# Kernel tuning notes

Hardware: AMD Instinct MI355X
Metric: run time of the kernel (lower is better)

The kernel has to match this reference:

```python
import jax, jax.numpy as jnp
import numpy as np

EPS = 1e-5
NEG_SLOPE = 0.2  # PyG GATConv default leaky_relu slope


def group_norm(x, w, b, groups):
    # x: [N, C] treated as batch of N samples, GroupNorm over channel groups
    N, C = x.shape
    xg = x.reshape(N, groups, C // groups)
    mu = xg.mean(-1, keepdims=True)
    var = ((xg - mu) ** 2).mean(-1, keepdims=True)
    xn = ((xg - mu) / jnp.sqrt(var + EPS)).reshape(N, C)
    return xn * w + b


def gat_conv(x, src, dst, W, a_src, a_dst, bias, n_nodes):
    # PyG GATConv, heads=1, concat=False, self-loops already appended to src/dst
    h = x @ W.T                                    # [N, C]
    alpha_src = h @ a_src                          # [N]
    alpha_dst = h @ a_dst                          # [N]
    e = jax.nn.leaky_relu(alpha_src[src] + alpha_dst[dst], NEG_SLOPE)  # [E]
    # segment softmax over edges grouped by destination node
    m = jax.ops.segment_max(e, dst, num_segments=n_nodes)
    ex = jnp.exp(e - m[dst])
    s = jax.ops.segment_sum(ex, dst, num_segments=n_nodes)
    alpha = ex / (s[dst] + 1e-16)                  # [E]
    out = jax.ops.segment_sum(h[src] * alpha[:, None], dst, num_segments=n_nodes)
    return out + bias


def setup_inputs() -> dict:
    key = jax.random.key(0)
    ks = jax.random.split(key, 32)
    N, E = 40000, 640000
    C_IN, C_OUT = 256, 512
    H = C_OUT // 2  # 256

    def xavier(k, shape):
        fan_in, fan_out = shape[1], shape[0]
        lim = np.sqrt(6.0 / (fan_in + fan_out))
        return jax.random.uniform(k, shape, jnp.float32, -lim, lim)

    inp = {
        "x": jax.random.normal(ks[0], (N, C_IN), jnp.float32),
        "edge_index": jax.random.randint(ks[1], (2, E), 0, N, jnp.int64),
        # pre_norm (GroupNorm(C_IN//8, C_IN))
        "pre_w": jnp.ones((C_IN,), jnp.float32),
        "pre_b": jnp.zeros((C_IN,), jnp.float32),
        # lin1: C_IN -> H
        "lin1_w": xavier(ks[2], (H, C_IN)),
        "lin1_b": jnp.zeros((H,), jnp.float32),
        "n1_w": jnp.ones((H,), jnp.float32),
        "n1_b": jnp.zeros((H,), jnp.float32),
        # GATConv 1 (H -> H, heads=1)
        "g1_w": xavier(ks[3], (H, H)),
        "g1_asrc": jax.random.normal(ks[4], (H,), jnp.float32) * 0.1,
        "g1_adst": jax.random.normal(ks[5], (H,), jnp.float32) * 0.1,
        "g1_b": jnp.zeros((H,), jnp.float32),
        "n2_w": jnp.ones((H,), jnp.float32),
        "n2_b": jnp.zeros((H,), jnp.float32),
        # GATConv 2
        "g2_w": xavier(ks[6], (H, H)),
        "g2_asrc": jax.random.normal(ks[7], (H,), jnp.float32) * 0.1,
        "g2_adst": jax.random.normal(ks[8], (H,), jnp.float32) * 0.1,
        "g2_b": jnp.zeros((H,), jnp.float32),
        "n3_w": jnp.ones((H,), jnp.float32),
        "n3_b": jnp.zeros((H,), jnp.float32),
        # lin2: H -> C_OUT
        "lin2_w": xavier(ks[9], (C_OUT, H)),
        "lin2_b": jnp.zeros((C_OUT,), jnp.float32),
        # skip_conv: C_IN -> C_OUT (in != out, so skip is applied)
        "skip_w": xavier(ks[10], (C_OUT, C_IN)),
        "skip_b": jnp.zeros((C_OUT,), jnp.float32),
    }
    return inp


def reference(x, edge_index, pre_w, pre_b, lin1_w, lin1_b, n1_w, n1_b,
              g1_w, g1_asrc, g1_adst, g1_b, n2_w, n2_b,
              g2_w, g2_asrc, g2_adst, g2_b, n3_w, n3_b,
              lin2_w, lin2_b, skip_w, skip_b):
    N, C_IN = x.shape
    H = lin1_w.shape[0]
    # add self loops (PyG GATConv default add_self_loops=True)
    loops = jnp.arange(N, dtype=edge_index.dtype)
    src = jnp.concatenate([edge_index[0], loops])
    dst = jnp.concatenate([edge_index[1], loops])

    y = jax.nn.elu(group_norm(x, pre_w, pre_b, C_IN // 8))
    y = y @ lin1_w.T + lin1_b
    y = jax.nn.elu(group_norm(y, n1_w, n1_b, H // 8))
    y = gat_conv(y, src, dst, g1_w, g1_asrc, g1_adst, g1_b, N)
    y = jax.nn.elu(group_norm(y, n2_w, n2_b, H // 8))
    y = gat_conv(y, src, dst, g2_w, g2_asrc, g2_adst, g2_b, N)
    y = jax.nn.elu(group_norm(y, n3_w, n3_b, H // 8))
    y = y @ lin2_w.T + lin2_b
    x_skip = x @ skip_w.T + skip_b  # in_channels != out_channels
    return x_skip + y
```

## Files before the change

### kernel.cpp

```cpp
#include <hip/hip_runtime.h>
#include <hip/hip_bf16.h>


typedef __bf16 bf16x8 __attribute__((ext_vector_type(8)));
typedef float floatx4 __attribute__((ext_vector_type(4)));

__device__ __forceinline__ __hip_bfloat16 f2b(float f) { return __float2bfloat16(f); }
__device__ __forceinline__ float bits2f(unsigned u) { return __uint_as_float(u << 16); }

__device__ __forceinline__ bf16x8 cvt8(const float* p) {
  float4 a = *(const float4*)p, b = *(const float4*)(p + 4);
  bf16x8 r;
  r[0] = (__bf16)a.x; r[1] = (__bf16)a.y; r[2] = (__bf16)a.z; r[3] = (__bf16)a.w;
  r[4] = (__bf16)b.x; r[5] = (__bf16)b.y; r[6] = (__bf16)b.z; r[7] = (__bf16)b.w;
  return r;
}

__global__ __launch_bounds__(256) void conv_w_k(
    const float* __restrict__ s0, const float* __restrict__ s1,
    const float* __restrict__ s2, const float* __restrict__ s3,
    const float* __restrict__ s4, __hip_bfloat16* __restrict__ d) {
  int i = (blockIdx.x * 256 + threadIdx.x) * 4;
  if (i >= 458752) return;
  const float* s; int off;
  if      (i < 65536)  { s = s0; off = 0; }
  else if (i < 131072) { s = s1; off = 65536; }
  else if (i < 196608) { s = s2; off = 131072; }
  else if (i < 327680) { s = s3; off = 196608; }
  else                 { s = s4; off = 327680; }
  float4 v = *(const float4*)(s + (i - off));
  union { ushort4 u; __hip_bfloat16 h[4]; } st;
  st.h[0] = f2b(v.x); st.h[1] = f2b(v.y); st.h[2] = f2b(v.z); st.h[3] = f2b(v.w);
  *(ushort4*)(d + i) = st.u;
}

__global__ __launch_bounds__(256) void gn_elu_k(
    const float* __restrict__ x, const float* __restrict__ w, const float* __restrict__ b,
    __hip_bfloat16* __restrict__ o, __hip_bfloat16* __restrict__ xb, int ng) {
  int g = blockIdx.x * 256 + threadIdx.x;
  if (g >= ng) return;
  int gi = g & 31;
  size_t basei = (size_t)g * 8;
  float4 u0 = *(const float4*)(x + basei), u1 = *(const float4*)(x + basei + 4);
  float f[8] = {u0.x, u0.y, u0.z, u0.w, u1.x, u1.y, u1.z, u1.w};
  if (xb) {
    union { uint4 u; __hip_bfloat16 h[8]; } xs;
#pragma unroll
    for (int i = 0; i < 8; i++) xs.h[i] = f2b(f[i]);
    *(uint4*)(xb + basei) = xs.u;
  }
  float mu = 0.f;
#pragma unroll
  for (int i = 0; i < 8; i++) mu += f[i];
  mu *= 0.125f;
  float var = 0.f;
#pragma unroll
  for (int i = 0; i < 8; i++) { float d = f[i] - mu; var += d * d; }
  float inv = rsqrtf(var * 0.125f + 1e-5f);
  union { uint4 u; __hip_bfloat16 h[8]; } st;
#pragma unroll
  for (int i = 0; i < 8; i++) {
    float vv = (f[i] - mu) * inv * w[gi * 8 + i] + b[gi * 8 + i];
    vv = (vv > 0.f) ? vv : (__expf(vv) - 1.f);
    st.h[i] = f2b(vv);
  }
  *(uint4*)(o + basei) = st.u;
}

template <int MODE>
__global__ __launch_bounds__(256, 3) void gemm_t(
    const __hip_bfloat16* __restrict__ A, const __hip_bfloat16* __restrict__ A2,
    const float* __restrict__ Af32,
    const __hip_bfloat16* __restrict__ W, const __hip_bfloat16* __restrict__ W2,
    const float* __restrict__ bias, const float* __restrict__ bias2,
    const float* __restrict__ gnw, const float* __restrict__ gnb,
    const float* __restrict__ avs, const float* __restrict__ avd,
    __hip_bfloat16* __restrict__ outB, float* __restrict__ outF,
    float* __restrict__ asrc, float* __restrict__ adst, int Nc, int Mreal) {
  const int tid = threadIdx.x;
  const int wn = tid >> 6, lane = tid & 63;
  const int l16 = lane & 15, quad = lane >> 4;
  const int rows0 = blockIdx.y * 64;
  const int col0 = blockIdx.x * 256;
  const int srow = tid >> 2, skc = (tid & 3) * 8;
  __shared__ __align__(16) __hip_bfloat16 sA[2][64 * 32];
  __shared__ __align__(16) __hip_bfloat16 sB[2][256 * 32];
  __shared__ float sRed[2][64][4];
  const int loA = tid * 8;

  floatx4 acc[4][4];
#pragma unroll
  for (int a = 0; a < 4; ++a)
#pragma unroll
    for (int b = 0; b < 4; ++b) acc[a][b] = (floatx4){0.f, 0.f, 0.f, 0.f};

  const int NK = (MODE >= 2) ? 16 : 8;
  uint4 pa, pb[4];
  pa = *(const uint4*)(A + (size_t)(rows0 + srow) * 256 + skc);
#pragma unroll
  for (int h = 0; h < 4; ++h)
    pb[h] = *(const uint4*)(W + (size_t)(col0 + srow + h * 64) * 256 + skc);
  *(uint4*)(&sA[0][loA]) = pa;
#pragma unroll
  for (int h = 0; h < 4; ++h) *(uint4*)(&sB[0][loA + h * 2048]) = pb[h];
  __syncthreads();

#pragma unroll
  for (int kt = 0; kt < NK; ++kt) {
    const int cur = kt & 1, nxt = cur ^ 1;
    const int ktn = kt + 1;
    const bool nsec = (MODE >= 2) && (ktn >= 8);
    const bool nstageA = (ktn < NK) && !(MODE == 3 && nsec);
    if (ktn < NK) {
      const int kkn = (ktn & 7) * 32;
      const __hip_bfloat16* Wb = nsec ? W2 : W;
      if (nstageA) {
        const __hip_bfloat16* Ab = (MODE == 2 && nsec) ? A2 : A;
        pa = *(const uint4*)(Ab + (size_t)(rows0 + srow) * 256 + kkn + skc);
      }
#pragma unroll
      for (int h = 0; h < 4; ++h)
        pb[h] = *(const uint4*)(Wb + (size_t)(col0 + srow + h * 64) * 256 + kkn + skc);
    }
    bf16x8 af[4], bfr[4];
    if (MODE == 3 && kt >= 8) {
      const int kk = (kt & 7) * 32;
#pragma unroll
      for (int ri = 0; ri < 4; ++ri) {
        int row = min(rows0 + ri * 16 + l16, Mreal - 1);
        af[ri] = cvt8(Af32 + (size_t)row * 256 + kk + quad * 8);
      }
    } else {
#pragma unroll
      for (int ri = 0; ri < 4; ++ri)
        af[ri] = *(const bf16x8*)(&sA[cur][(ri * 16 + l16) * 32 + quad * 8]);
    }
#pragma unroll
    for (int ci = 0; ci < 4; ++ci)
      bfr[ci] = *(const bf16x8*)(&sB[cur][(wn * 64 + ci * 16 + l16) * 32 + quad * 8]);
#pragma unroll
    for (int ri = 0; ri < 4; ++ri)
#pragma unroll
      for (int ci = 0; ci < 4; ++ci)
        acc[ri][ci] = __builtin_amdgcn_mfma_f32_16x16x32_bf16(af[ri], bfr[ci], acc[ri][ci], 0, 0, 0);
    if (ktn < NK) {
      if (nstageA) *(uint4*)(&sA[nxt][loA]) = pa;
#pragma unroll
      for (int h = 0; h < 4; ++h) *(uint4*)(&sB[nxt][loA + h * 2048]) = pb[h];
    }
    __syncthreads();
  }

  if (MODE == 0) {
#pragma unroll
    for (int ri = 0; ri < 4; ++ri)
#pragma unroll
      for (int ci = 0; ci < 4; ++ci) {
        int col = col0 + wn * 64 + ci * 16 + l16;
        float bs = bias[col], gw = gnw[col], gb = gnb[col];
#pragma unroll
        for (int i = 0; i < 4; ++i) {
          float v = acc[ri][ci][i] + bs;
          float s = v;
          s += __shfl_xor(s, 1, 64); s += __shfl_xor(s, 2, 64); s += __shfl_xor(s, 4, 64);
          float mu = s * 0.125f, d = v - mu;
          float q = d * d;
          q += __shfl_xor(q, 1, 64); q += __shfl_xor(q, 2, 64); q += __shfl_xor(q, 4, 64);
          float r = d * rsqrtf(q * 0.125f + 1e-5f) * gw + gb;
          r = (r > 0.f) ? r : (__expf(r) - 1.f);
          outB[(size_t)(rows0 + ri * 16 + quad * 4 + i) * 256 + col] = f2b(r);
        }
      }
  } else if (MODE == 1) {
#pragma unroll
    for (int ri = 0; ri < 4; ++ri) {
      float ps[4] = {0.f, 0.f, 0.f, 0.f}, pd[4] = {0.f, 0.f, 0.f, 0.f};
#pragma unroll
      for (int ci = 0; ci < 4; ++ci) {
        int col = col0 + wn * 64 + ci * 16 + l16;
        float wsv = avs[col], wdv = avd[col];
#pragma unroll
        for (int i = 0; i < 4; ++i) {
          float v = acc[ri][ci][i];
          outB[(size_t)(rows0 + ri * 16 + quad * 4 + i) * 256 + col] = f2b(v);
          ps[i] += v * wsv; pd[i] += v * wdv;
        }
      }
#pragma unroll
      for (int i = 0; i < 4; ++i) {
        ps[i] += __shfl_xor(ps[i], 1, 64); ps[i] += __shfl_xor(ps[i], 2, 64);
        ps[i] += __shfl_xor(ps[i], 4, 64); ps[i] += __shfl_xor(ps[i], 8, 64);
        pd[i] += __shfl_xor(pd[i], 1, 64); pd[i] += __shfl_xor(pd[i], 2, 64);
        pd[i] += __shfl_xor(pd[i], 4, 64); pd[i] += __shfl_xor(pd[i], 8, 64);
        if (l16 == 0) {
          int r = ri * 16 + quad * 4 + i;
          sRed[0][r][wn] = ps[i];
          sRed[1][r][wn] = pd[i];
        }
      }
    }
    __syncthreads();
    if (tid < 128) {
      int arr = tid >> 6, r = tid & 63;
      float v = sRed[arr][r][0] + sRed[arr][r][1] + sRed[arr][r][2] + sRed[arr][r][3];
      (arr ? adst : asrc)[rows0 + r] = v;
    }
  } else {
#pragma unroll
    for (int ri = 0; ri < 4; ++ri)
#pragma unroll
      for (int ci = 0; ci < 4; ++ci) {
        int col = col0 + wn * 64 + ci * 16 + l16;
        float bs = bias[col] + bias2[col];
#pragma unroll
        for (int i = 0; i < 4; ++i) {
          int row = rows0 + ri * 16 + quad * 4 + i;
          if (row < Mreal) outF[(size_t)row * Nc + col] = acc[ri][ci][i] + bs;
        }
      }
  }
}

__global__ void zero_k(int* p, int n) {
  int i = blockIdx.x * blockDim.x + threadIdx.x;
  if (i < n) p[i] = 0;
}

__global__ void count_deg_k(const int* __restrict__ ei, int E, int NN, int* __restrict__ counts) {
  int e = blockIdx.x * blockDim.x + threadIdx.x;
  if (e >= E + NN) return;
  int d = (e < E) ? ei[E + e] : (e - E);
  if ((unsigned)d >= (unsigned)NN) d = 0;
  atomicAdd(&counts[d], 1);
}

__global__ __launch_bounds__(1024) void scan_blk_k(const int* __restrict__ counts,
                                                   int* __restrict__ indptr,
                                                   int* __restrict__ bsums, int NN) {
  __shared__ int wsum[16];
  int t = threadIdx.x, idx = blockIdx.x * 1024 + t;
  int lane = t & 63, wid = t >> 6;
  int v = (idx < NN) ? counts[idx] : 0;
  int s = v;
#pragma unroll
  for (int off = 1; off < 64; off <<= 1) {
    int u = __shfl_up(s, off, 64);
    if (lane >= off) s += u;
  }
  if (lane == 63) wsum[wid] = s;
  __syncthreads();
  if (t == 0) {
    int run = 0;
#pragma unroll
    for (int i = 0; i < 16; i++) { int u = wsum[i]; wsum[i] = run; run += u; }
    bsums[blockIdx.x] = run;
  }
  __syncthreads();
  if (idx < NN) indptr[idx] = s - v + wsum[wid];
}

__global__ void scan_top_k(int* bsums, int nb) {
  if (threadIdx.x == 0) {
    int run = 0;
    for (int i = 0; i < nb; i++) { int t = bsums[i]; bsums[i] = run; run += t; }
  }
}

__global__ __launch_bounds__(1024) void scan_add_k(int* __restrict__ indptr, int* __restrict__ fill,
                                                   const int* __restrict__ bsums, int NN, int ET) {
  int idx = blockIdx.x * 1024 + threadIdx.x;
  if (idx < NN) {
    int v = indptr[idx] + bsums[blockIdx.x];
    indptr[idx] = v; fill[idx] = v;
  }
  if (idx == 0) indptr[NN] = ET;
}

__global__ void fill_csr_k(const int* __restrict__ ei, int E, int NN,
                           int* __restrict__ fill, int* __restrict__ csr, int ET) {
  int e = blockIdx.x * blockDim.x + threadIdx.x;
  if (e >= E + NN) return;
  int s, d;
  if (e < E) { s = ei[e]; d = ei[E + e]; } else { s = e - E; d = e - E; }
  if ((unsigned)d >= (unsigned)NN) d = 0;
  if ((unsigned)s >= (unsigned)NN) s = 0;
  int slot = atomicAdd(&fill[d], 1);
  if ((unsigned)slot < (unsigned)ET) csr[slot] = s;
}

__global__ __launch_bounds__(256) void gat_agg_gn_k(
    const __hip_bfloat16* __restrict__ h, const float* __restrict__ asrc,
    const float* __restrict__ adst, const int* __restrict__ indptr,
    const int* __restrict__ csr, const float* __restrict__ gbias,
    const float* __restrict__ gnw, const float* __restrict__ gnb,
    __hip_bfloat16* __restrict__ outp, int NN, int ET) {
  int n = blockIdx.x * 4 + (threadIdx.x >> 6);
  if (n >= NN) return;
  int lane = threadIdx.x & 63;
  int half = lane >> 5, l32 = lane & 31;
  int beg = indptr[n], end = indptr[n + 1];
  beg = max(0, min(beg, ET));
  end = max(beg, min(end, ET));
  int deg = end - beg;
  float adn = adst[n];
  float a[8] = {0.f, 0.f, 0.f, 0.f, 0.f, 0.f, 0.f, 0.f};
  float lw = 0.f;

  for (int cb = 0; cb < deg; cb += 64) {
    int j = cb + lane;
    int sid = 0; float w = 0.f;
    if (j < deg) {
      sid = csr[beg + j];
      if ((unsigned)sid >= (unsigned)NN) sid = 0;
      float e = asrc[sid] + adn;
      e = (e > 0.f) ? e : 0.2f * e;
      e = fminf(fmaxf(e, -60.f), 60.f);
      w = __expf(e);
    }
    lw += w;
    int cnt = min(64, deg - cb);
    for (int t = 0; t < cnt; t += 2) {
      int idx = t + half;
      int s = __shfl(sid, idx, 64);
      float wt = __shfl(w, idx, 64);
      uint4 u = *(const uint4*)(h + (size_t)s * 256 + l32 * 8);
      a[0] += wt * bits2f(u.x & 0xffffu); a[1] += wt * bits2f(u.x >> 16);
      a[2] += wt * bits2f(u.y & 0xffffu); a[3] += wt * bits2f(u.y >> 16);
      a[4] += wt * bits2f(u.z & 0xffffu); a[5] += wt * bits2f(u.z >> 16);
      a[6] += wt * bits2f(u.w & 0xffffu); a[7] += wt * bits2f(u.w >> 16);
    }
  }
#pragma unroll
  for (int i = 0; i < 8; ++i) a[i] += __shfl_xor(a[i], 32, 64);
#pragma unroll
  for (int m = 32; m >= 1; m >>= 1) lw += __shfl_xor(lw, m, 64);
  if (half == 0) {
    float inv = 1.f / (lw + 1e-16f);
    int c0 = l32 * 8;
    float v[8], mu = 0.f;
#pragma unroll
    for (int i = 0; i < 8; ++i) { v[i] = a[i] * inv + gbias[c0 + i]; mu += v[i]; }
    mu *= 0.125f;
    float q = 0.f;
#pragma unroll
    for (int i = 0; i < 8; ++i) { float d = v[i] - mu; q += d * d; }
    float rs = rsqrtf(q * 0.125f + 1e-5f);
    union { uint4 u; __hip_bfloat16 b[8]; } st;
#pragma unroll
    for (int i = 0; i < 8; ++i) {
      float r = (v[i] - mu) * rs * gnw[c0 + i] + gnb[c0 + i];
      r = (r > 0.f) ? r : (__expf(r) - 1.f);
      st.b[i] = f2b(r);
    }
    *(uint4*)(outp + (size_t)n * 256 + c0) = st.u;
  }
}

extern "C" void kernel_launch(void* const* d_in, const int* in_sizes, int n_in,
                              void* d_out, int out_size, void* d_ws, size_t ws_size,
                              hipStream_t stream) {
  const float* x      = (const float*)d_in[0];
  const int*   ei     = (const int*)d_in[1];
  const float* pre_w  = (const float*)d_in[2];
  const float* pre_b  = (const float*)d_in[3];
  const float* lin1_b = (const float*)d_in[5];
  const float* n1_w   = (const float*)d_in[6];
  const float* n1_b   = (const float*)d_in[7];
  const float* g1_as  = (const float*)d_in[9];
  const float* g1_ad  = (const float*)d_in[10];
  const float* g1_b   = (const float*)d_in[11];
  const float* n2_w   = (const float*)d_in[12];
  const float* n2_b   = (const float*)d_in[13];
  const float* g2_as  = (const float*)d_in[15];
  const float* g2_ad  = (const float*)d_in[16];
  const float* g2_b   = (const float*)d_in[17];
  const float* n3_w   = (const float*)d_in[18];
  const float* n3_b   = (const float*)d_in[19];
  const float* lin2_b = (const float*)d_in[21];
  const float* skip_b = (const float*)d_in[23];
  float* out = (float*)d_out;

  const int C_IN  = in_sizes[2];
  const int NN    = in_sizes[0] / C_IN;
  const int E     = in_sizes[1] / 2;
  const int ET    = E + NN;
  const int C_OUT = in_sizes[21];
  const int NP    = (NN + 127) & ~127;

  __hip_bfloat16* D0 = (__hip_bfloat16*)d_out;
  __hip_bfloat16* D1 = D0 + (size_t)NP * 256;

  char* basep = (char*)d_ws;
  size_t o = 0;
  auto alloc = [&](size_t bytes) { size_t r = o; o += (bytes + 255) & ~(size_t)255; return r; };
  __hip_bfloat16* Y      = (__hip_bfloat16*)(basep + alloc((size_t)NP * 256 * 2));
  __hip_bfloat16* Wcat   = (__hip_bfloat16*)(basep + alloc((size_t)458752 * 2));
  float*          asrc   = (float*)(basep + alloc((size_t)NP * 4));
  float*          adst   = (float*)(basep + alloc((size_t)NP * 4));
  int*            indptr = (int*)(basep + alloc((size_t)(NN + 1) * 4));
  int*            counts = (int*)(basep + alloc((size_t)NN * 4));
  int*            fill   = (int*)(basep + alloc((size_t)NN * 4));
  int*            bsums  = (int*)(basep + alloc(256));
  int*            csr    = (int*)(basep + alloc((size_t)ET * 4));
  size_t base_need = o;
  size_t xb_need = ((size_t)NP * 256 * 2 + 255) & ~(size_t)255;
  const bool use_xb = (ws_size >= base_need + xb_need);
  __hip_bfloat16* xb = use_xb ? (__hip_bfloat16*)(basep + alloc(xb_need)) : nullptr;

  __hip_bfloat16* Wlin1 = Wcat;
  __hip_bfloat16* Wg1   = Wcat + 65536;
  __hip_bfloat16* Wg2   = Wcat + 131072;
  __hip_bfloat16* Wlin2 = Wcat + 196608;
  __hip_bfloat16* Wskip = Wcat + 327680;

  dim3 blk(256);
  const int nb = (NN + 1023) / 1024;

  conv_w_k<<<(458752 / 4 + 255) / 256, blk, 0, stream>>>(
      (const float*)d_in[4], (const float*)d_in[8], (const float*)d_in[14],
      (const float*)d_in[20], (const float*)d_in[22], Wcat);
  zero_k<<<(NN + 255) / 256, blk, 0, stream>>>(counts, NN);
  count_deg_k<<<(ET + 255) / 256, blk, 0, stream>>>(ei, E, NN, counts);
  scan_blk_k<<<nb, 1024, 0, stream>>>(counts, indptr, bsums, NN);
  scan_top_k<<<1, 64, 0, stream>>>(bsums, nb);
  scan_add_k<<<nb, 1024, 0, stream>>>(indptr, fill, bsums, NN, ET);
  fill_csr_k<<<(ET + 255) / 256, blk, 0, stream>>>(ei, E, NN, fill, csr, ET);

  gn_elu_k<<<(NN * 32 + 255) / 256, blk, 0, stream>>>(x, pre_w, pre_b, D0, xb, NN * 32);
  gemm_t<0><<<dim3(1, NP / 64), blk, 0, stream>>>(D0, nullptr, nullptr, Wlin1, nullptr,
      lin1_b, nullptr, n1_w, n1_b, nullptr, nullptr, Y, nullptr, nullptr, nullptr, 256, NN);
  gemm_t<1><<<dim3(1, NP / 64), blk, 0, stream>>>(Y, nullptr, nullptr, Wg1, nullptr,
      nullptr, nullptr, nullptr, nullptr, g1_as, g1_ad, D0, nullptr, asrc, adst, 256, NN);
  gat_agg_gn_k<<<NN / 4, blk, 0, stream>>>(D0, asrc, adst, indptr, csr, g1_b, n2_w, n2_b, D1, NN, ET);
  gemm_t<1><<<dim3(1, NP / 64), blk, 0, stream>>>(D1, nullptr, nullptr, Wg2, nullptr,
      nullptr, nullptr, nullptr, nullptr, g2_as, g2_ad, D0, nullptr, asrc, adst, 256, NN);
  gat_agg_gn_k<<<NN / 4, blk, 0, stream>>>(D0, asrc, adst, indptr, csr, g2_b, n3_w, n3_b, Y, NN, ET);
  if (use_xb) {
    gemm_t<2><<<dim3(C_OUT / 256, NP / 64), blk, 0, stream>>>(Y, xb, nullptr, Wlin2, Wskip,
        lin2_b, skip_b, nullptr, nullptr, nullptr, nullptr, nullptr, out, nullptr, nullptr, C_OUT, NN);
  } else {
    gemm_t<3><<<dim3(C_OUT / 256, NP / 64), blk, 0, stream>>>(Y, nullptr, x, Wlin2, Wskip,
        lin2_b, skip_b, nullptr, nullptr, nullptr, nullptr, nullptr, out, nullptr, nullptr, C_OUT, NN);
  }
}
```

Baseline: 440.7 us.

## Split GAT aggregation into alpha pass and channel-blocked gather over blocked h layout

The GAT projection GEMM now writes h in a channel-blocked layout (8 blocks of 32 channels, each contiguous over rows). A new alpha kernel precomputes per-edge exp weights packed with source ids, plus the inverse softmax denominator per node. The aggregation kernel then runs one block per node group and channel block, gathering 64-byte rows so each channel slice stays small enough to stay cache-resident. This trades an extra kernel launch and an 8-byte-per-edge write and read for better gather locality, with GroupNorm reduced over 4-lane groups.

```diff
diff --git a/kernel.cpp b/kernel.cpp
--- a/kernel.cpp
+++ b/kernel.cpp
@@ -172,17 +172,20 @@
         }
       }
   } else if (MODE == 1) {
+    const int NPl = (Mreal + 127) & ~127;
 #pragma unroll
     for (int ri = 0; ri < 4; ++ri) {
       float ps[4] = {0.f, 0.f, 0.f, 0.f}, pd[4] = {0.f, 0.f, 0.f, 0.f};
 #pragma unroll
       for (int ci = 0; ci < 4; ++ci) {
         int col = col0 + wn * 64 + ci * 16 + l16;
+        int cbk = col >> 5, chin = col & 31;
         float wsv = avs[col], wdv = avd[col];
 #pragma unroll
         for (int i = 0; i < 4; ++i) {
           float v = acc[ri][ci][i];
-          outB[(size_t)(rows0 + ri * 16 + quad * 4 + i) * 256 + col] = f2b(v);
+          int row = rows0 + ri * 16 + quad * 4 + i;
+          outB[(size_t)cbk * NPl * 32 + (size_t)row * 32 + chin] = f2b(v);
           ps[i] += v * wsv; pd[i] += v * wdv;
         }
       }
@@ -288,71 +291,101 @@
   if ((unsigned)slot < (unsigned)ET) csr[slot] = s;
 }
 
-__global__ __launch_bounds__(256) void gat_agg_gn_k(
-    const __hip_bfloat16* __restrict__ h, const float* __restrict__ asrc,
-    const float* __restrict__ adst, const int* __restrict__ indptr,
-    const int* __restrict__ csr, const float* __restrict__ gbias,
-    const float* __restrict__ gnw, const float* __restrict__ gnb,
-    __hip_bfloat16* __restrict__ outp, int NN, int ET) {
+__global__ __launch_bounds__(256) void alpha_k(
+    const float* __restrict__ asrc, const float* __restrict__ adst,
+    const int* __restrict__ indptr, const int* __restrict__ csr,
+    unsigned long long* __restrict__ ew, float* __restrict__ lwinv, int NN, int ET) {
   int n = blockIdx.x * 4 + (threadIdx.x >> 6);
   if (n >= NN) return;
   int lane = threadIdx.x & 63;
-  int half = lane >> 5, l32 = lane & 31;
   int beg = indptr[n], end = indptr[n + 1];
   beg = max(0, min(beg, ET));
   end = max(beg, min(end, ET));
   int deg = end - beg;
   float adn = adst[n];
-  float a[8] = {0.f, 0.f, 0.f, 0.f, 0.f, 0.f, 0.f, 0.f};
   float lw = 0.f;
-
-  for (int cb = 0; cb < deg; cb += 64) {
-    int j = cb + lane;
-    int sid = 0; float w = 0.f;
+  for (int c0 = 0; c0 < deg; c0 += 64) {
+    int j = c0 + lane;
     if (j < deg) {
-      sid = csr[beg + j];
+      int sid = csr[beg + j];
       if ((unsigned)sid >= (unsigned)NN) sid = 0;
       float e = asrc[sid] + adn;
       e = (e > 0.f) ? e : 0.2f * e;
       e = fminf(fmaxf(e, -60.f), 60.f);
-      w = __expf(e);
-    }
-    lw += w;
-    int cnt = min(64, deg - cb);
-    for (int t = 0; t < cnt; t += 2) {
-      int idx = t + half;
-      int s = __shfl(sid, idx, 64);
-      float wt = __shfl(w, idx, 64);
-      uint4 u = *(const uint4*)(h + (size_t)s * 256 + l32 * 8);
-      a[0] += wt * bits2f(u.x & 0xffffu); a[1] += wt * bits2f(u.x >> 16);
-      a[2] += wt * bits2f(u.y & 0xffffu); a[3] += wt * bits2f(u.y >> 16);
-      a[4] += wt * bits2f(u.z & 0xffffu); a[5] += wt * bits2f(u.z >> 16);
-      a[6] += wt * bits2f(u.w & 0xffffu); a[7] += wt * bits2f(u.w >> 16);
-    }
-  }
-#pragma unroll
-  for (int i = 0; i < 8; ++i) a[i] += __shfl_xor(a[i], 32, 64);
+      float w = __expf(e);
+      ew[beg + j] = (unsigned)sid | ((unsigned long long)__float_as_uint(w) << 32);
+      lw += w;
+    }
+  }
 #pragma unroll
   for (int m = 32; m >= 1; m >>= 1) lw += __shfl_xor(lw, m, 64);
-  if (half == 0) {
-    float inv = 1.f / (lw + 1e-16f);
-    int c0 = l32 * 8;
-    float v[8], mu = 0.f;
-#pragma unroll
-    for (int i = 0; i < 8; ++i) { v[i] = a[i] * inv + gbias[c0 + i]; mu += v[i]; }
-    mu *= 0.125f;
-    float q = 0.f;
-#pragma unroll
-    for (int i = 0; i < 8; ++i) { float d = v[i] - mu; q += d * d; }
+  if (lane == 0) lwinv[n] = 1.f / (lw + 1e-16f);
+}
+
+__global__ __launch_bounds__(256) void gat_pass_k(
+    const __hip_bfloat16* __restrict__ hb, const unsigned long long* __restrict__ ew,
+    const float* __restrict__ lwinv, const int* __restrict__ indptr,
+    const float* __restrict__ gbias, const float* __restrict__ gnw,
+    const float* __restrict__ gnb, __hip_bfloat16* __restrict__ outp,
+    int NN, int NP, int ET) {
+  int bid = blockIdx.x;
+  int cbk = bid & 7;
+  int n = (bid >> 3) * 4 + (threadIdx.x >> 6);
+  if (n >= NN) return;
+  int lane = threadIdx.x & 63;
+  int qw = lane >> 4, l16 = lane & 15;
+  const __hip_bfloat16* hc = hb + (size_t)cbk * NP * 32;
+  int beg = indptr[n], end = indptr[n + 1];
+  beg = max(0, min(beg, ET));
+  end = max(beg, min(end, ET));
+  int deg = end - beg;
+  float a0 = 0.f, a1 = 0.f;
+
+  for (int c0 = 0; c0 < deg; c0 += 64) {
+    int j = c0 + lane;
+    int sid = 0; float w = 0.f;
+    if (j < deg) {
+      unsigned long long pv = __builtin_nontemporal_load(ew + beg + j);
+      sid = (int)(unsigned)pv;
+      w = __uint_as_float((unsigned)(pv >> 32));
+    }
+    int cnt = min(64, deg - c0);
+    for (int t = 0; t < cnt; t += 16) {
+      int i0 = t + qw, i1 = t + 4 + qw, i2 = t + 8 + qw, i3 = t + 12 + qw;
+      int s0 = __shfl(sid, i0, 64), s1 = __shfl(sid, i1, 64),
+          s2 = __shfl(sid, i2, 64), s3 = __shfl(sid, i3, 64);
+      float w0 = __shfl(w, i0, 64), w1 = __shfl(w, i1, 64),
+            w2 = __shfl(w, i2, 64), w3 = __shfl(w, i3, 64);
+      unsigned u0 = *(const unsigned*)(hc + (size_t)s0 * 32 + l16 * 2);
+      unsigned u1 = *(const unsigned*)(hc + (size_t)s1 * 32 + l16 * 2);
+      unsigned u2 = *(const unsigned*)(hc + (size_t)s2 * 32 + l16 * 2);
+      unsigned u3 = *(const unsigned*)(hc + (size_t)s3 * 32 + l16 * 2);
+      a0 += w0 * bits2f(u0 & 0xffffu); a1 += w0 * bits2f(u0 >> 16);
+      a0 += w1 * bits2f(u1 & 0xffffu); a1 += w1 * bits2f(u1 >> 16);
+      a0 += w2 * bits2f(u2 & 0xffffu); a1 += w2 * bits2f(u2 >> 16);
+      a0 += w3 * bits2f(u3 & 0xffffu); a1 += w3 * bits2f(u3 >> 16);
+    }
+  }
+  a0 += __shfl_xor(a0, 16, 64); a0 += __shfl_xor(a0, 32, 64);
+  a1 += __shfl_xor(a1, 16, 64); a1 += __shfl_xor(a1, 32, 64);
+  if (qw == 0) {
+    float inv = lwinv[n];
+    int ch = cbk * 32 + l16 * 2;
+    float v0 = a0 * inv + gbias[ch], v1 = a1 * inv + gbias[ch + 1];
+    float s = v0 + v1;
+    s += __shfl_xor(s, 1, 64); s += __shfl_xor(s, 2, 64);
+    float mu = s * 0.125f;
+    float d0 = v0 - mu, d1 = v1 - mu;
+    float q = d0 * d0 + d1 * d1;
+    q += __shfl_xor(q, 1, 64); q += __shfl_xor(q, 2, 64);
     float rs = rsqrtf(q * 0.125f + 1e-5f);
-    union { uint4 u; __hip_bfloat16 b[8]; } st;
-#pragma unroll
-    for (int i = 0; i < 8; ++i) {
-      float r = (v[i] - mu) * rs * gnw[c0 + i] + gnb[c0 + i];
-      r = (r > 0.f) ? r : (__expf(r) - 1.f);
-      st.b[i] = f2b(r);
-    }
-    *(uint4*)(outp + (size_t)n * 256 + c0) = st.u;
+    float r0 = d0 * rs * gnw[ch] + gnb[ch];
+    r0 = (r0 > 0.f) ? r0 : (__expf(r0) - 1.f);
+    float r1 = d1 * rs * gnw[ch + 1] + gnb[ch + 1];
+    r1 = (r1 > 0.f) ? r1 : (__expf(r1) - 1.f);
+    union { unsigned u; __hip_bfloat16 h[2]; } st;
+    st.h[0] = f2b(r0); st.h[1] = f2b(r1);
+    *(unsigned*)(outp + (size_t)n * 256 + ch) = st.u;
   }
 }
 
@@ -402,6 +435,8 @@
   int*            fill   = (int*)(basep + alloc((size_t)NN * 4));
   int*            bsums  = (int*)(basep + alloc(256));
   int*            csr    = (int*)(basep + alloc((size_t)ET * 4));
+  unsigned long long* ew = (unsigned long long*)(basep + alloc((size_t)ET * 8));
+  float*          lwinv  = (float*)(basep + alloc((size_t)NN * 4));
   size_t base_need = o;
   size_t xb_need = ((size_t)NP * 256 * 2 + 255) & ~(size_t)255;
   const bool use_xb = (ws_size >= base_need + xb_need);
@@ -415,6 +450,7 @@
 
   dim3 blk(256);
   const int nb = (NN + 1023) / 1024;
+  const int ngrp = (NN + 3) / 4;
 
   conv_w_k<<<(458752 / 4 + 255) / 256, blk, 0, stream>>>(
       (const float*)d_in[4], (const float*)d_in[8], (const float*)d_in[14],
@@ -431,10 +467,12 @@
       lin1_b, nullptr, n1_w, n1_b, nullptr, nullptr, Y, nullptr, nullptr, nullptr, 256, NN);
   gemm_t<1><<<dim3(1, NP / 64), blk, 0, stream>>>(Y, nullptr, nullptr, Wg1, nullptr,
       nullptr, nullptr, nullptr, nullptr, g1_as, g1_ad, D0, nullptr, asrc, adst, 256, NN);
-  gat_agg_gn_k<<<NN / 4, blk, 0, stream>>>(D0, asrc, adst, indptr, csr, g1_b, n2_w, n2_b, D1, NN, ET);
+  alpha_k<<<ngrp, blk, 0, stream>>>(asrc, adst, indptr, csr, ew, lwinv, NN, ET);
+  gat_pass_k<<<ngrp * 8, blk, 0, stream>>>(D0, ew, lwinv, indptr, g1_b, n2_w, n2_b, D1, NN, NP, ET);
   gemm_t<1><<<dim3(1, NP / 64), blk, 0, stream>>>(D1, nullptr, nullptr, Wg2, nullptr,
       nullptr, nullptr, nullptr, nullptr, g2_as, g2_ad, D0, nullptr, asrc, adst, 256, NN);
-  gat_agg_gn_k<<<NN / 4, blk, 0, stream>>>(D0, asrc, adst, indptr, csr, g2_b, n3_w, n3_b, Y, NN, ET);
+  alpha_k<<<ngrp, blk, 0, stream>>>(asrc, adst, indptr, csr, ew, lwinv, NN, ET);
+  gat_pass_k<<<ngrp * 8, blk, 0, stream>>>(D0, ew, lwinv, indptr, g2_b, n3_w, n3_b, Y, NN, NP, ET);
   if (use_xb) {
     gemm_t<2><<<dim3(C_OUT / 256, NP / 64), blk, 0, stream>>>(Y, xb, nullptr, Wlin2, Wskip,
         lin2_b, skip_b, nullptr, nullptr, nullptr, nullptr, nullptr, out, nullptr, nullptr, C_OUT, NN);
```

New measurement: 609.1 us. 1.38x slower.
